# Kernel tuning notes

Hardware: AMD Instinct MI355X
Metric: run time of the kernel (lower is better)

The kernel has to match this reference:

```python
import jax, jax.numpy as jnp
import numpy as np

N = 50000
E = 1_600_000
H = 128          # hidden_dim
HEADS = 4
PH = H // 2      # platform embedding dim = 64
LRELU_SLOPE = 0.2
BN_EPS = 1e-5


def _lin_init(key, fan_in, fan_out):
    return jax.random.normal(key, (fan_in, fan_out), jnp.float32) / np.sqrt(fan_in)


def setup_inputs() -> dict:
    key = jax.random.key(0)
    ks = jax.random.split(key, 32)
    inp = {}
    inp["x"] = jax.random.normal(ks[0], (N, 10), jnp.float32)
    inp["edge_index"] = jax.random.randint(ks[1], (2, E), 0, N, jnp.int32)
    inp["platform_x"] = jax.random.normal(ks[2], (1, 4), jnp.float32)
    # node encoder
    inp["node_W"] = _lin_init(ks[3], 10, H); inp["node_b"] = jnp.zeros((H,))
    # platform encoder
    inp["plat_W"] = _lin_init(ks[4], 4, PH); inp["plat_b"] = jnp.zeros((PH,))
    # GAT layers: W [in, heads*out], att vectors [1, heads, out], bias [heads*out]
    inp["g1_W"] = _lin_init(ks[5], H, H)
    inp["g1_asrc"] = jax.random.normal(ks[6], (1, HEADS, H // HEADS)) * 0.1
    inp["g1_adst"] = jax.random.normal(ks[7], (1, HEADS, H // HEADS)) * 0.1
    inp["g1_b"] = jnp.zeros((H,))
    inp["g2_W"] = _lin_init(ks[8], H, H)
    inp["g2_asrc"] = jax.random.normal(ks[9], (1, HEADS, H // HEADS)) * 0.1
    inp["g2_adst"] = jax.random.normal(ks[10], (1, HEADS, H // HEADS)) * 0.1
    inp["g2_b"] = jnp.zeros((H,))
    inp["g3_W"] = _lin_init(ks[11], H, H)
    inp["g3_asrc"] = jax.random.normal(ks[12], (1, 1, H)) * 0.1
    inp["g3_adst"] = jax.random.normal(ks[13], (1, 1, H)) * 0.1
    inp["g3_b"] = jnp.zeros((H,))
    # BatchNorm (eval mode: running_mean=0, running_var=1)
    for i, k in zip((1, 2, 3), (ks[14], ks[15], ks[16])):
        inp[f"bn{i}_g"] = jnp.ones((H,)) + 0.1 * jax.random.normal(k, (H,))
        inp[f"bn{i}_b"] = jnp.zeros((H,))
    # classifier: 192 -> 128 -> 64 -> 3
    inp["c1_W"] = _lin_init(ks[17], H + PH, H); inp["c1_b"] = jnp.zeros((H,))
    inp["c2_W"] = _lin_init(ks[18], H, PH);     inp["c2_b"] = jnp.zeros((PH,))
    inp["c3_W"] = _lin_init(ks[19], PH, 3);     inp["c3_b"] = jnp.zeros((3,))
    return inp


def gat_conv(x, src, dst, W, a_src, a_dst, b, heads, out_dim, n):
    # PyG GATConv (eval, self-loops already appended): gather -> edge score ->
    # segment softmax over destination -> scatter-add.
    h = (x @ W).reshape(n, heads, out_dim)              # [N, heads, out]
    al_s = jnp.sum(h * a_src, axis=-1)                  # [N, heads]
    al_d = jnp.sum(h * a_dst, axis=-1)                  # [N, heads]
    e = jax.nn.leaky_relu(al_s[src] + al_d[dst], LRELU_SLOPE)  # [E, heads]
    m = jax.ops.segment_max(e, dst, num_segments=n)
    m = jnp.where(jnp.isfinite(m), m, 0.0)
    ex = jnp.exp(e - m[dst])
    s = jax.ops.segment_sum(ex, dst, num_segments=n)
    alpha = ex / (s[dst] + 1e-16)                       # [E, heads]
    out = jax.ops.segment_sum(alpha[:, :, None] * h[src], dst, num_segments=n)
    return out.reshape(n, heads * out_dim) + b


def bn_eval(x, g, b):
    # running_mean=0, running_var=1 -> x / sqrt(1+eps) * g + b
    return x * (g / np.sqrt(1.0 + BN_EPS)) + b


def reference(x, edge_index, platform_x, node_W, node_b, plat_W, plat_b,
              g1_W, g1_asrc, g1_adst, g1_b, g2_W, g2_asrc, g2_adst, g2_b,
              g3_W, g3_asrc, g3_adst, g3_b, bn1_g, bn1_b, bn2_g, bn2_b,
              bn3_g, bn3_b, c1_W, c1_b, c2_W, c2_b, c3_W, c3_b):
    n = x.shape[0]
    loops = jnp.arange(n, dtype=edge_index.dtype)
    src = jnp.concatenate([edge_index[0], loops])
    dst = jnp.concatenate([edge_index[1], loops])

    h = jax.nn.relu(x @ node_W + node_b)
    h = gat_conv(h, src, dst, g1_W, g1_asrc, g1_adst, g1_b, HEADS, H // HEADS, n)
    h = jax.nn.relu(bn_eval(h, bn1_g, bn1_b))
    h = gat_conv(h, src, dst, g2_W, g2_asrc, g2_adst, g2_b, HEADS, H // HEADS, n)
    h = jax.nn.relu(bn_eval(h, bn2_g, bn2_b))
    h = gat_conv(h, src, dst, g3_W, g3_asrc, g3_adst, g3_b, 1, H, n)
    h = jax.nn.relu(bn_eval(h, bn3_g, bn3_b))

    p = jax.nn.relu(platform_x @ plat_W + plat_b)       # [1, PH]
    p = jnp.broadcast_to(p[0:1], (n, PH))
    h = jnp.concatenate([h, p], axis=1)                 # [N, H+PH]

    h = jax.nn.relu(h @ c1_W + c1_b)
    h = jax.nn.relu(h @ c2_W + c2_b)
    return h @ c3_W + c3_b                              # [N, 3]
```

## Files before the change

kernel.cpp:

```cpp
#include <hip/hip_runtime.h>
#include <hip/hip_bf16.h>
#include <hip/hip_fp16.h>

#define LRELU 0.2f
#define BN_INVS 0.99999500003749968f

__global__ __launch_bounds__(256) void k_initdeg(int* deg, int n) {
    int i = blockIdx.x * 256 + threadIdx.x;
    if (i < n) deg[i] = 1;
}

__global__ __launch_bounds__(256) void k_count(const int* __restrict__ ei, int* deg, int E) {
    int e = blockIdx.x * 256 + threadIdx.x;
    if (e < E) atomicAdd(&deg[ei[E + e]], 1);
}

__global__ __launch_bounds__(1024) void k_scan1(const int* __restrict__ deg, int* row_ptr,
                                                int* bsum, int n) {
    __shared__ int sm[1024];
    int t = threadIdx.x, g = blockIdx.x * 1024 + t;
    sm[t] = (g < n) ? deg[g] : 0;
    __syncthreads();
    for (int off = 1; off < 1024; off <<= 1) {
        int x = (t >= off) ? sm[t - off] : 0;
        __syncthreads();
        sm[t] += x;
        __syncthreads();
    }
    if (g < n) row_ptr[g + 1] = sm[t];
    if (t == 1023) bsum[blockIdx.x] = sm[t];
}

__global__ void k_scan2(const int* bsum, int* boff, int nb) {
    if (threadIdx.x == 0 && blockIdx.x == 0) {
        int s = 0;
        for (int i = 0; i < nb; ++i) { boff[i] = s; s += bsum[i]; }
    }
}

__global__ __launch_bounds__(1024) void k_scan3(int* row_ptr, const int* boff, int n) {
    int g = blockIdx.x * 1024 + threadIdx.x;
    if (g < n) row_ptr[g + 1] += boff[blockIdx.x];
    if (g == 0) row_ptr[0] = 0;
}

__global__ __launch_bounds__(256) void k_cursor(const int* __restrict__ rp, int* cur, int n) {
    int i = blockIdx.x * 256 + threadIdx.x;
    if (i < n) cur[i] = rp[i];
}

__global__ __launch_bounds__(256) void k_scatter(const int* __restrict__ ei, int* cur, int* col,
                                                 int E, int n) {
    int g = blockIdx.x & 7;
    int W = (n + 7) >> 3;
    int lo = g * W;
    int hi = min(n, lo + W);
    int nb = gridDim.x >> 3;
    int bi = blockIdx.x >> 3;
    int stride = nb * 256;
    for (int t = bi * 256 + threadIdx.x; t < E; t += stride) {
        int d = ei[E + t];
        if (d >= lo && d < hi) {
            int p = atomicAdd(&cur[d], 1);
            col[p] = ei[t];
        }
    }
    for (int v = lo + bi * 256 + threadIdx.x; v < hi; v += stride) {
        int p = atomicAdd(&cur[v], 1);
        col[p] = v;
    }
}

__global__ __launch_bounds__(256) void k_node_enc(const float* __restrict__ x,
                                                  const float* __restrict__ W,
                                                  const float* __restrict__ b,
                                                  float* __restrict__ h, int n) {
    __shared__ float Ws[1280];
    __shared__ float bs[128];
    for (int i = threadIdx.x; i < 1280; i += 256) Ws[i] = W[i];
    if (threadIdx.x < 128) bs[threadIdx.x] = b[threadIdx.x];
    __syncthreads();
    int idx = blockIdx.x * 256 + threadIdx.x;
    if (idx >= n * 32) return;
    int v = idx >> 5, q = idx & 31;
    float xr[10];
#pragma unroll
    for (int i = 0; i < 10; ++i) xr[i] = x[v * 10 + i];
    float o[4];
#pragma unroll
    for (int j = 0; j < 4; ++j) {
        int c = q * 4 + j;
        float s = bs[c];
#pragma unroll
        for (int i = 0; i < 10; ++i) s += xr[i] * Ws[i * 128 + c];
        o[j] = fmaxf(s, 0.f);
    }
    *(float4*)(h + (size_t)v * 128 + q * 4) = make_float4(o[0], o[1], o[2], o[3]);
}

template <int M, bool ADD_BIAS, bool RELU, bool HALF_OUT = false>
__global__ __launch_bounds__(256) void k_gemm128(const float* __restrict__ A,
                                                 const float* __restrict__ B,
                                                 const float* __restrict__ bias,
                                                 float* __restrict__ C, int n) {
    constexpr int NG = M / 64;
    __shared__ float AsT[32][133];
    __shared__ float Bs[32][M];
    int tid = threadIdx.x;
    int row0 = blockIdx.x * 128;
    int ct = tid & 15, rt = tid >> 4;
    float4 acc[8][NG];
#pragma unroll
    for (int i = 0; i < 8; ++i)
#pragma unroll
        for (int g = 0; g < NG; ++g) acc[i][g] = make_float4(0.f, 0.f, 0.f, 0.f);

    for (int kc = 0; kc < 128; kc += 32) {
#pragma unroll
        for (int i = 0; i < 4; ++i) {
            int f = tid + i * 256;
            int r = f >> 3;
            int kq = (f & 7) * 4;
            float4 v = make_float4(0.f, 0.f, 0.f, 0.f);
            int gr = row0 + r;
            if (gr < n) v = *(const float4*)(A + (size_t)gr * 128 + kc + kq);
            AsT[kq + 0][r] = v.x;
            AsT[kq + 1][r] = v.y;
            AsT[kq + 2][r] = v.z;
            AsT[kq + 3][r] = v.w;
        }
#pragma unroll
        for (int i = 0; i < M / 32; ++i) {
            int f = tid + i * 256;
            int r = f / (M / 4), c4 = (f % (M / 4)) * 4;
            *(float4*)(&Bs[r][c4]) = *(const float4*)(B + (size_t)(kc + r) * M + c4);
        }
        __syncthreads();
#pragma unroll
        for (int k = 0; k < 32; ++k) {
            float4 a0 = *(const float4*)(&AsT[k][rt * 8]);
            float4 a1 = *(const float4*)(&AsT[k][rt * 8 + 4]);
            float av[8] = {a0.x, a0.y, a0.z, a0.w, a1.x, a1.y, a1.z, a1.w};
#pragma unroll
            for (int g = 0; g < NG; ++g) {
                float4 bv = *(const float4*)(&Bs[k][g * 64 + ct * 4]);
#pragma unroll
                for (int i = 0; i < 8; ++i) {
                    acc[i][g].x += av[i] * bv.x;
                    acc[i][g].y += av[i] * bv.y;
                    acc[i][g].z += av[i] * bv.z;
                    acc[i][g].w += av[i] * bv.w;
                }
            }
        }
        __syncthreads();
    }
    float4 bb[NG];
    if (ADD_BIAS) {
#pragma unroll
        for (int g = 0; g < NG; ++g) bb[g] = *(const float4*)(bias + g * 64 + ct * 4);
    }
#pragma unroll
    for (int i = 0; i < 8; ++i) {
        int gr = row0 + rt * 8 + i;
        if (gr < n) {
#pragma unroll
            for (int g = 0; g < NG; ++g) {
                float4 v = acc[i][g];
                if (ADD_BIAS) {
                    v.x += bb[g].x; v.y += bb[g].y; v.z += bb[g].z; v.w += bb[g].w;
                }
                if (RELU) {
                    v.x = fmaxf(v.x, 0.f); v.y = fmaxf(v.y, 0.f);
                    v.z = fmaxf(v.z, 0.f); v.w = fmaxf(v.w, 0.f);
                }
                if (HALF_OUT) {
                    __half hb[4];
                    hb[0] = __float2half(v.x);
                    hb[1] = __float2half(v.y);
                    hb[2] = __float2half(v.z);
                    hb[3] = __float2half(v.w);
                    __half* C16 = reinterpret_cast<__half*>(C);
                    *(ushort4*)(C16 + (size_t)gr * M + g * 64 + ct * 4) = *(ushort4*)hb;
                } else {
                    *(float4*)(C + (size_t)gr * M + g * 64 + ct * 4) = v;
                }
            }
        }
    }
}

template <int HEADS>
__global__ __launch_bounds__(256) void k_al(const __half* __restrict__ hw,
                                            const float* __restrict__ asrc,
                                            const float* __restrict__ adst,
                                            float* __restrict__ al_s, float* __restrict__ al_d,
                                            int n) {
    int wid = (blockIdx.x * 256 + threadIdx.x) >> 6;
    int l = threadIdx.x & 63;
    if (wid >= n) return;
    unsigned raw = *(const unsigned*)(hw + (size_t)wid * 128 + 2 * l);
    __half2 hp = *reinterpret_cast<__half2*>(&raw);
    float2 hv = __half22float2(hp);
    int c0 = 2 * l;
    if (HEADS == 4) {
        int h = l >> 4, dd = c0 & 31;
        float s = hv.x * asrc[h * 32 + dd] + hv.y * asrc[h * 32 + dd + 1];
        float d = hv.x * adst[h * 32 + dd] + hv.y * adst[h * 32 + dd + 1];
#pragma unroll
        for (int off = 1; off < 16; off <<= 1) {
            s += __shfl_xor(s, off);
            d += __shfl_xor(d, off);
        }
        if ((l & 15) == 0) {
            al_s[wid * 4 + h] = s;
            al_d[wid * 4 + h] = d;
        }
    } else {
        float s = hv.x * asrc[c0] + hv.y * asrc[c0 + 1];
        float d = hv.x * adst[c0] + hv.y * adst[c0 + 1];
#pragma unroll
        for (int off = 1; off < 64; off <<= 1) {
            s += __shfl_xor(s, off);
            d += __shfl_xor(d, off);
        }
        if (l == 0) {
            al_s[wid] = s;
            al_d[wid] = d;
        }
    }
}

template <int HEADS>
__global__ __launch_bounds__(256) void k_softagg(const int* __restrict__ rp,
                                                 const int* __restrict__ col,
                                                 const float* __restrict__ al_s,
                                                 const float* __restrict__ al_d,
                                                 const __half* __restrict__ hw,
                                                 const float* __restrict__ gb,
                                                 const float* __restrict__ bng,
                                                 const float* __restrict__ bnb,
                                                 float* __restrict__ hout, int n) {
    constexpr int CAP = 128;
    __shared__ int ss[4][CAP];
    __shared__ __align__(16) float se[4][CAP * HEADS];
    int v = (blockIdx.x * 256 + threadIdx.x) >> 6;
    int l = threadIdx.x & 63;
    int w = threadIdx.x >> 6;
    if (v >= n) return;
    int start = rp[v], end = rp[v + 1];

    float ad[HEADS], m[HEADS], s[HEADS];
#pragma unroll
    for (int h = 0; h < HEADS; ++h) {
        ad[h] = al_d[v * HEADS + h];
        m[h] = -1e30f;
        s[h] = 0.f;
    }

    for (int p = start + l; p < end; p += 64) {
        int src = col[p];
        float eh[HEADS];
        if (HEADS == 4) {
            float4 t4 = *(const float4*)(al_s + (size_t)src * 4);
            eh[0] = t4.x; eh[1] = t4.y; eh[2] = t4.z; eh[3] = t4.w;
        } else {
            eh[0] = al_s[src];
        }
#pragma unroll
        for (int h = 0; h < HEADS; ++h) {
            float e = eh[h] + ad[h];
            eh[h] = (e >= 0.f) ? e : LRELU * e;
        }
        int idx = p - start;
        if (idx < CAP) {
            ss[w][idx] = src;
            if (HEADS == 4)
                *(float4*)(&se[w][idx * 4]) = make_float4(eh[0], eh[1], eh[2], eh[3]);
            else
                se[w][idx] = eh[0];
        }
#pragma unroll
        for (int h = 0; h < HEADS; ++h) {
            float nm = fmaxf(m[h], eh[h]);
            s[h] = s[h] * __expf(m[h] - nm) + __expf(eh[h] - nm);
            m[h] = nm;
        }
    }
#pragma unroll
    for (int off = 1; off < 64; off <<= 1) {
#pragma unroll
        for (int h = 0; h < HEADS; ++h) {
            float om = __shfl_xor(m[h], off), os = __shfl_xor(s[h], off);
            float nm = fmaxf(m[h], om);
            s[h] = s[h] * __expf(m[h] - nm) + os * __expf(om - nm);
            m[h] = nm;
        }
    }
    float inv[HEADS];
#pragma unroll
    for (int h = 0; h < HEADS; ++h) inv[h] = 1.f / (s[h] + 1e-16f);

    int ew = l >> 5;
    int li = l & 31;
    int c4 = 4 * li;
    int hd = (HEADS == 4) ? (li >> 3) : 0;
    float mh = m[hd], invh = inv[hd], adh = ad[hd];
    float4 acc = make_float4(0.f, 0.f, 0.f, 0.f);

    int p = start + ew;
    for (; p + 2 < end; p += 4) {
        int i0 = p - start, i1 = i0 + 2;
        int s0, s1;
        float e0, e1;
        if (i0 < CAP) {
            s0 = ss[w][i0];
            e0 = (HEADS == 4) ? se[w][i0 * 4 + hd] : se[w][i0];
        } else {
            s0 = col[p];
            float t = al_s[(size_t)s0 * HEADS + hd] + adh;
            e0 = (t >= 0.f) ? t : LRELU * t;
        }
        if (i1 < CAP) {
            s1 = ss[w][i1];
            e1 = (HEADS == 4) ? se[w][i1 * 4 + hd] : se[w][i1];
        } else {
            s1 = col[p + 2];
            float t = al_s[(size_t)s1 * HEADS + hd] + adh;
            e1 = (t >= 0.f) ? t : LRELU * t;
        }
        float a0 = __expf(e0 - mh);
        float a1 = __expf(e1 - mh);
        uint2 r0 = *(const uint2*)(hw + (size_t)s0 * 128 + c4);
        uint2 r1 = *(const uint2*)(hw + (size_t)s1 * 128 + c4);
        float2 f00 = __half22float2(*reinterpret_cast<__half2*>(&r0.x));
        float2 f01 = __half22float2(*reinterpret_cast<__half2*>(&r0.y));
        float2 f10 = __half22float2(*reinterpret_cast<__half2*>(&r1.x));
        float2 f11 = __half22float2(*reinterpret_cast<__half2*>(&r1.y));
        acc.x += a0 * f00.x + a1 * f10.x;
        acc.y += a0 * f00.y + a1 * f10.y;
        acc.z += a0 * f01.x + a1 * f11.x;
        acc.w += a0 * f01.y + a1 * f11.y;
    }
    if (p < end) {
        int i0 = p - start;
        int s0;
        float e0;
        if (i0 < CAP) {
            s0 = ss[w][i0];
            e0 = (HEADS == 4) ? se[w][i0 * 4 + hd] : se[w][i0];
        } else {
            s0 = col[p];
            float t = al_s[(size_t)s0 * HEADS + hd] + adh;
            e0 = (t >= 0.f) ? t : LRELU * t;
        }
        float a0 = __expf(e0 - mh);
        uint2 r0 = *(const uint2*)(hw + (size_t)s0 * 128 + c4);
        float2 f00 = __half22float2(*reinterpret_cast<__half2*>(&r0.x));
        float2 f01 = __half22float2(*reinterpret_cast<__half2*>(&r0.y));
        acc.x += a0 * f00.x;
        acc.y += a0 * f00.y;
        acc.z += a0 * f01.x;
        acc.w += a0 * f01.y;
    }
    acc.x += __shfl_xor(acc.x, 32);
    acc.y += __shfl_xor(acc.y, 32);
    acc.z += __shfl_xor(acc.z, 32);
    acc.w += __shfl_xor(acc.w, 32);

    if (l < 32) {
        float4 g4 = *(const float4*)(gb + c4);
        float4 bg = *(const float4*)(bng + c4);
        float4 bbv = *(const float4*)(bnb + c4);
        float4 o;
        o.x = fmaxf((acc.x * invh + g4.x) * (bg.x * BN_INVS) + bbv.x, 0.f);
        o.y = fmaxf((acc.y * invh + g4.y) * (bg.y * BN_INVS) + bbv.y, 0.f);
        o.z = fmaxf((acc.z * invh + g4.z) * (bg.z * BN_INVS) + bbv.z, 0.f);
        o.w = fmaxf((acc.w * invh + g4.w) * (bg.w * BN_INVS) + bbv.w, 0.f);
        *(float4*)(hout + (size_t)v * 128 + c4) = o;
    }
}

__global__ void k_pconst(const float* __restrict__ px, const float* __restrict__ pW,
                         const float* __restrict__ pb, const float* __restrict__ c1W,
                         const float* __restrict__ c1b, float* __restrict__ cvec) {
    __shared__ float p[64];
    int t = threadIdx.x;
    if (t < 64) {
        float s = pb[t];
#pragma unroll
        for (int i = 0; i < 4; ++i) s += px[i] * pW[i * 64 + t];
        p[t] = fmaxf(s, 0.f);
    }
    __syncthreads();
    if (t < 128) {
        float s = c1b[t];
#pragma unroll
        for (int j = 0; j < 64; ++j) s += p[j] * c1W[(128 + j) * 128 + t];
        cvec[t] = s;
    }
}

__global__ __launch_bounds__(256) void k_c3(const float* __restrict__ h5,
                                            const float* __restrict__ W,
                                            const float* __restrict__ b, float* __restrict__ out,
                                            int n) {
    __shared__ float Ws[192];
    __shared__ float bs[3];
    if (threadIdx.x < 192) Ws[threadIdx.x] = W[threadIdx.x];
    if (threadIdx.x < 3) bs[threadIdx.x] = b[threadIdx.x];
    __syncthreads();
    int v = blockIdx.x * 256 + threadIdx.x;
    if (v >= n) return;
    float a0 = bs[0], a1 = bs[1], a2 = bs[2];
#pragma unroll
    for (int k4 = 0; k4 < 16; ++k4) {
        float4 xv = *(const float4*)(h5 + (size_t)v * 64 + k4 * 4);
        int k = k4 * 4;
        a0 += xv.x * Ws[k * 3 + 0] + xv.y * Ws[k * 3 + 3] + xv.z * Ws[k * 3 + 6] + xv.w * Ws[k * 3 + 9];
        a1 += xv.x * Ws[k * 3 + 1] + xv.y * Ws[k * 3 + 4] + xv.z * Ws[k * 3 + 7] + xv.w * Ws[k * 3 + 10];
        a2 += xv.x * Ws[k * 3 + 2] + xv.y * Ws[k * 3 + 5] + xv.z * Ws[k * 3 + 8] + xv.w * Ws[k * 3 + 11];
    }
    out[v * 3 + 0] = a0;
    out[v * 3 + 1] = a1;
    out[v * 3 + 2] = a2;
}

extern "C" void kernel_launch(void* const* d_in, const int* in_sizes, int n_in,
                              void* d_out, int out_size, void* d_ws, size_t ws_size,
                              hipStream_t stream) {
    const float* x      = (const float*)d_in[0];
    const int*   ei     = (const int*)d_in[1];
    const float* px     = (const float*)d_in[2];
    const float* node_W = (const float*)d_in[3];
    const float* node_b = (const float*)d_in[4];
    const float* plat_W = (const float*)d_in[5];
    const float* plat_b = (const float*)d_in[6];
    const float* g1_W = (const float*)d_in[7];
    const float* g1_as = (const float*)d_in[8];
    const float* g1_ad = (const float*)d_in[9];
    const float* g1_b = (const float*)d_in[10];
    const float* g2_W = (const float*)d_in[11];
    const float* g2_as = (const float*)d_in[12];
    const float* g2_ad = (const float*)d_in[13];
    const float* g2_b = (const float*)d_in[14];
    const float* g3_W = (const float*)d_in[15];
    const float* g3_as = (const float*)d_in[16];
    const float* g3_ad = (const float*)d_in[17];
    const float* g3_b = (const float*)d_in[18];
    const float* bn1_g = (const float*)d_in[19];
    const float* bn1_b = (const float*)d_in[20];
    const float* bn2_g = (const float*)d_in[21];
    const float* bn2_b = (const float*)d_in[22];
    const float* bn3_g = (const float*)d_in[23];
    const float* bn3_b = (const float*)d_in[24];
    const float* c1_W = (const float*)d_in[25];
    const float* c1_b = (const float*)d_in[26];
    const float* c2_W = (const float*)d_in[27];
    const float* c2_b = (const float*)d_in[28];
    const float* c3_W = (const float*)d_in[29];
    const float* c3_b = (const float*)d_in[30];

    const int N = in_sizes[0] / 10;
    const int E = in_sizes[1] / 2;
    const int ET = E + N;

    char* w = (char*)d_ws;
    auto alloc = [&](size_t bytes) {
        void* p = (void*)w;
        w += (bytes + 255) & ~(size_t)255;
        return p;
    };
    int*   col     = (int*)alloc((size_t)ET * 4);
    int*   deg     = (int*)alloc((size_t)N * 4);
    int*   row_ptr = (int*)alloc((size_t)(N + 1) * 4);
    int*   bsum    = (int*)alloc(256 * 4);
    int*   boff    = (int*)alloc(256 * 4);
    float* al_s    = (float*)alloc((size_t)N * 4 * 4);
    float* al_d    = (float*)alloc((size_t)N * 4 * 4);
    float* bufA    = (float*)alloc((size_t)N * 128 * 4);
    float* bufB    = (float*)alloc((size_t)N * 128 * 4);
    float* cvec    = (float*)alloc(128 * 4);
    float* out     = (float*)d_out;
    __half* h16    = (__half*)bufB;

    const int NB = (N + 1023) / 1024;

    k_initdeg<<<(N + 255) / 256, 256, 0, stream>>>(deg, N);
    k_count<<<(E + 255) / 256, 256, 0, stream>>>(ei, deg, E);
    k_scan1<<<NB, 1024, 0, stream>>>(deg, row_ptr, bsum, N);
    k_scan2<<<1, 64, 0, stream>>>(bsum, boff, NB);
    k_scan3<<<NB, 1024, 0, stream>>>(row_ptr, boff, N);
    k_cursor<<<(N + 255) / 256, 256, 0, stream>>>(row_ptr, deg, N);
    k_scatter<<<832, 256, 0, stream>>>(ei, deg, col, E, N);

    k_node_enc<<<(N * 32 + 255) / 256, 256, 0, stream>>>(x, node_W, node_b, bufA, N);

    const int gGemm = (N + 127) / 128;
    const int gWave = (N * 64 + 255) / 256;

    k_gemm128<128, false, false, true><<<gGemm, 256, 0, stream>>>(bufA, g1_W, nullptr, (float*)h16, N);
    k_al<4><<<gWave, 256, 0, stream>>>(h16, g1_as, g1_ad, al_s, al_d, N);
    k_softagg<4><<<gWave, 256, 0, stream>>>(row_ptr, col, al_s, al_d, h16, g1_b, bn1_g, bn1_b, bufA, N);

    k_gemm128<128, false, false, true><<<gGemm, 256, 0, stream>>>(bufA, g2_W, nullptr, (float*)h16, N);
    k_al<4><<<gWave, 256, 0, stream>>>(h16, g2_as, g2_ad, al_s, al_d, N);
    k_softagg<4><<<gWave, 256, 0, stream>>>(row_ptr, col, al_s, al_d, h16, g2_b, bn2_g, bn2_b, bufA, N);

    k_gemm128<128, false, false, true><<<gGemm, 256, 0, stream>>>(bufA, g3_W, nullptr, (float*)h16, N);
    k_al<1><<<gWave, 256, 0, stream>>>(h16, g3_as, g3_ad, al_s, al_d, N);
    k_softagg<1><<<gWave, 256, 0, stream>>>(row_ptr, col, al_s, al_d, h16, g3_b, bn3_g, bn3_b, bufA, N);

    k_pconst<<<1, 128, 0, stream>>>(px, plat_W, plat_b, c1_W, c1_b, cvec);

    k_gemm128<128, true, true><<<gGemm, 256, 0, stream>>>(bufA, c1_W, cvec, bufB, N);
    k_gemm128<64, true, true><<<gGemm, 256, 0, stream>>>(bufB, c2_W, c2_b, bufA, N);
    k_c3<<<(N + 255) / 256, 256, 0, stream>>>(bufA, c3_W, c3_b, out, N);
}
```

Measured before the change: 738.7 us.

## Add fast path for low-degree nodes with precomputed softmax weights and wider gathers

For nodes whose degree fits in the shared-memory cache (average degree is about 33, so nearly all), the softmax becomes two passes: a max reduction, then exponentials written back to shared memory and summed. The online rescaling exps and per-lane exp recomputation during aggregation are gone. Aggregation now has each lane gather 8 halves (16 bytes), with 4 edges in flight per wave instead of 2, followed by a two-level shuffle reduction. High-degree nodes take a simplified path without caching. The scatter kernel's grid size is also quadrupled.

```diff
diff --git a/kernel.cpp b/kernel.cpp
--- a/kernel.cpp
+++ b/kernel.cpp
@@ -249,13 +249,107 @@
     int w = threadIdx.x >> 6;
     if (v >= n) return;
     int start = rp[v], end = rp[v + 1];
-
-    float ad[HEADS], m[HEADS], s[HEADS];
+    int deg = end - start;
+
+    float ad[HEADS], m[HEADS], s[HEADS], inv[HEADS];
 #pragma unroll
     for (int h = 0; h < HEADS; ++h) {
         ad[h] = al_d[v * HEADS + h];
         m[h] = -1e30f;
         s[h] = 0.f;
+    }
+
+    if (deg <= CAP) {
+        for (int p = start + l; p < end; p += 64) {
+            int src = col[p];
+            float eh[HEADS];
+            if (HEADS == 4) {
+                float4 t4 = *(const float4*)(al_s + (size_t)src * 4);
+                eh[0] = t4.x; eh[1] = t4.y; eh[2] = t4.z; eh[3] = t4.w;
+            } else {
+                eh[0] = al_s[src];
+            }
+#pragma unroll
+            for (int h = 0; h < HEADS; ++h) {
+                float e = eh[h] + ad[h];
+                eh[h] = (e >= 0.f) ? e : LRELU * e;
+                m[h] = fmaxf(m[h], eh[h]);
+            }
+            int idx = p - start;
+            ss[w][idx] = src;
+            if (HEADS == 4)
+                *(float4*)(&se[w][idx * 4]) = make_float4(eh[0], eh[1], eh[2], eh[3]);
+            else
+                se[w][idx] = eh[0];
+        }
+#pragma unroll
+        for (int off = 1; off < 64; off <<= 1)
+#pragma unroll
+            for (int h = 0; h < HEADS; ++h) m[h] = fmaxf(m[h], __shfl_xor(m[h], off));
+
+        for (int idx = l; idx < deg; idx += 64) {
+            if (HEADS == 4) {
+                float4 e4 = *(float4*)(&se[w][idx * 4]);
+                e4.x = __expf(e4.x - m[0]);
+                e4.y = __expf(e4.y - m[1]);
+                e4.z = __expf(e4.z - m[2]);
+                e4.w = __expf(e4.w - m[3]);
+                *(float4*)(&se[w][idx * 4]) = e4;
+                s[0] += e4.x; s[1] += e4.y; s[2] += e4.z; s[3] += e4.w;
+            } else {
+                float a = __expf(se[w][idx] - m[0]);
+                se[w][idx] = a;
+                s[0] += a;
+            }
+        }
+#pragma unroll
+        for (int off = 1; off < 64; off <<= 1)
+#pragma unroll
+            for (int h = 0; h < HEADS; ++h) s[h] += __shfl_xor(s[h], off);
+#pragma unroll
+        for (int h = 0; h < HEADS; ++h) inv[h] = 1.f / (s[h] + 1e-16f);
+
+        int qe = l >> 4;
+        int li = l & 15;
+        int c8 = li * 8;
+        int hd = (HEADS == 4) ? (li >> 2) : 0;
+        float invh = inv[hd];
+        float acc[8] = {0.f, 0.f, 0.f, 0.f, 0.f, 0.f, 0.f, 0.f};
+        for (int p = start + qe; p < end; p += 4) {
+            int idx = p - start;
+            int s0 = ss[w][idx];
+            float a0 = (HEADS == 4) ? se[w][idx * 4 + hd] : se[w][idx];
+            uint4 r = *(const uint4*)(hw + (size_t)s0 * 128 + c8);
+            float2 f0 = __half22float2(*reinterpret_cast<__half2*>(&r.x));
+            float2 f1 = __half22float2(*reinterpret_cast<__half2*>(&r.y));
+            float2 f2 = __half22float2(*reinterpret_cast<__half2*>(&r.z));
+            float2 f3 = __half22float2(*reinterpret_cast<__half2*>(&r.w));
+            acc[0] += a0 * f0.x; acc[1] += a0 * f0.y;
+            acc[2] += a0 * f1.x; acc[3] += a0 * f1.y;
+            acc[4] += a0 * f2.x; acc[5] += a0 * f2.y;
+            acc[6] += a0 * f3.x; acc[7] += a0 * f3.y;
+        }
+#pragma unroll
+        for (int j = 0; j < 8; ++j) {
+            acc[j] += __shfl_xor(acc[j], 16);
+            acc[j] += __shfl_xor(acc[j], 32);
+        }
+        if (l < 16) {
+#pragma unroll
+            for (int half = 0; half < 2; ++half) {
+                int c4 = c8 + half * 4;
+                float4 g4 = *(const float4*)(gb + c4);
+                float4 bg = *(const float4*)(bng + c4);
+                float4 bbv = *(const float4*)(bnb + c4);
+                float4 o;
+                o.x = fmaxf((acc[half * 4 + 0] * invh + g4.x) * (bg.x * BN_INVS) + bbv.x, 0.f);
+                o.y = fmaxf((acc[half * 4 + 1] * invh + g4.y) * (bg.y * BN_INVS) + bbv.y, 0.f);
+                o.z = fmaxf((acc[half * 4 + 2] * invh + g4.z) * (bg.z * BN_INVS) + bbv.z, 0.f);
+                o.w = fmaxf((acc[half * 4 + 3] * invh + g4.w) * (bg.w * BN_INVS) + bbv.w, 0.f);
+                *(float4*)(hout + (size_t)v * 128 + c4) = o;
+            }
+        }
+        return;
     }
 
     for (int p = start + l; p < end; p += 64) {
@@ -270,20 +364,9 @@
 #pragma unroll
         for (int h = 0; h < HEADS; ++h) {
             float e = eh[h] + ad[h];
-            eh[h] = (e >= 0.f) ? e : LRELU * e;
-        }
-        int idx = p - start;
-        if (idx < CAP) {
-            ss[w][idx] = src;
-            if (HEADS == 4)
-                *(float4*)(&se[w][idx * 4]) = make_float4(eh[0], eh[1], eh[2], eh[3]);
-            else
-                se[w][idx] = eh[0];
-        }
-#pragma unroll
-        for (int h = 0; h < HEADS; ++h) {
-            float nm = fmaxf(m[h], eh[h]);
-            s[h] = s[h] * __expf(m[h] - nm) + __expf(eh[h] - nm);
+            e = (e >= 0.f) ? e : LRELU * e;
+            float nm = fmaxf(m[h], e);
+            s[h] = s[h] * __expf(m[h] - nm) + __expf(e - nm);
             m[h] = nm;
         }
     }
@@ -297,7 +380,6 @@
             m[h] = nm;
         }
     }
-    float inv[HEADS];
 #pragma unroll
     for (int h = 0; h < HEADS; ++h) inv[h] = 1.f / (s[h] + 1e-16f);
 
@@ -307,53 +389,10 @@
     int hd = (HEADS == 4) ? (li >> 3) : 0;
     float mh = m[hd], invh = inv[hd], adh = ad[hd];
     float4 acc = make_float4(0.f, 0.f, 0.f, 0.f);
-
-    int p = start + ew;
-    for (; p + 2 < end; p += 4) {
-        int i0 = p - start, i1 = i0 + 2;
-        int s0, s1;
-        float e0, e1;
-        if (i0 < CAP) {
-            s0 = ss[w][i0];
-            e0 = (HEADS == 4) ? se[w][i0 * 4 + hd] : se[w][i0];
-        } else {
-            s0 = col[p];
-            float t = al_s[(size_t)s0 * HEADS + hd] + adh;
-            e0 = (t >= 0.f) ? t : LRELU * t;
-        }
-        if (i1 < CAP) {
-            s1 = ss[w][i1];
-            e1 = (HEADS == 4) ? se[w][i1 * 4 + hd] : se[w][i1];
-        } else {
-            s1 = col[p + 2];
-            float t = al_s[(size_t)s1 * HEADS + hd] + adh;
-            e1 = (t >= 0.f) ? t : LRELU * t;
-        }
-        float a0 = __expf(e0 - mh);
-        float a1 = __expf(e1 - mh);
-        uint2 r0 = *(const uint2*)(hw + (size_t)s0 * 128 + c4);
-        uint2 r1 = *(const uint2*)(hw + (size_t)s1 * 128 + c4);
-        float2 f00 = __half22float2(*reinterpret_cast<__half2*>(&r0.x));
-        float2 f01 = __half22float2(*reinterpret_cast<__half2*>(&r0.y));
-        float2 f10 = __half22float2(*reinterpret_cast<__half2*>(&r1.x));
-        float2 f11 = __half22float2(*reinterpret_cast<__half2*>(&r1.y));
-        acc.x += a0 * f00.x + a1 * f10.x;
-        acc.y += a0 * f00.y + a1 * f10.y;
-        acc.z += a0 * f01.x + a1 * f11.x;
-        acc.w += a0 * f01.y + a1 * f11.y;
-    }
-    if (p < end) {
-        int i0 = p - start;
-        int s0;
-        float e0;
-        if (i0 < CAP) {
-            s0 = ss[w][i0];
-            e0 = (HEADS == 4) ? se[w][i0 * 4 + hd] : se[w][i0];
-        } else {
-            s0 = col[p];
-            float t = al_s[(size_t)s0 * HEADS + hd] + adh;
-            e0 = (t >= 0.f) ? t : LRELU * t;
-        }
+    for (int p = start + ew; p < end; p += 2) {
+        int s0 = col[p];
+        float t = al_s[(size_t)s0 * HEADS + hd] + adh;
+        float e0 = (t >= 0.f) ? t : LRELU * t;
         float a0 = __expf(e0 - mh);
         uint2 r0 = *(const uint2*)(hw + (size_t)s0 * 128 + c4);
         float2 f00 = __half22float2(*reinterpret_cast<__half2*>(&r0.x));
@@ -367,7 +406,6 @@
     acc.y += __shfl_xor(acc.y, 32);
     acc.z += __shfl_xor(acc.z, 32);
     acc.w += __shfl_xor(acc.w, 32);
-
     if (l < 32) {
         float4 g4 = *(const float4*)(gb + c4);
         float4 bg = *(const float4*)(bng + c4);
@@ -492,7 +530,7 @@
     k_scan2<<<1, 64, 0, stream>>>(bsum, boff, NB);
     k_scan3<<<NB, 1024, 0, stream>>>(row_ptr, boff, N);
     k_cursor<<<(N + 255) / 256, 256, 0, stream>>>(row_ptr, deg, N);
-    k_scatter<<<832, 256, 0, stream>>>(ei, deg, col, E, N);
+    k_scatter<<<3328, 256, 0, stream>>>(ei, deg, col, E, N);
 
     k_node_enc<<<(N * 32 + 255) / 256, 256, 0, stream>>>(x, node_W, node_b, bufA, N);
 
```

Result: faster. 720.6 us (-2.4%).
